# Kernel tuning notes

Measured on AMD Instinct MI355X. Metric: run time of the kernel, lower is better.

## Reference

```python
import jax, jax.numpy as jnp
import numpy as np

FACTOR = 1.0
MARGIN = 0.5
NUM_CLASS = 19


def setup_inputs() -> dict:
    key = jax.random.key(0)
    k1, k2, k3 = jax.random.split(key, 3)
    B, C, H, W = 8, 256, 128, 128
    features = jax.random.normal(k1, (B, C, H, W), dtype=jnp.float32)
    labels = jax.random.randint(k2, (B, H, W), 0, NUM_CLASS, dtype=jnp.int32)
    prototypes = jax.random.normal(k3, (NUM_CLASS, C), dtype=jnp.float32)
    return {"features": features, "labels": labels, "prototypes": prototypes}


def reference(features, labels, prototypes):
    b, c, h, w = features.shape
    # flatten to [N, C] pixels and [N] labels (labels already at (h, w))
    feat = jnp.transpose(features, (0, 2, 3, 1)).reshape(-1, c)
    lab = labels.reshape(-1)
    # per-class mean via one-pass segment reduce (all classes present)
    sums = jax.ops.segment_sum(feat, lab, num_segments=NUM_CLASS)          # [K, C]
    counts = jax.ops.segment_sum(jnp.ones_like(lab, feat.dtype), lab,
                                 num_segments=NUM_CLASS)                   # [K]
    means = sums / jnp.maximum(counts, 1.0)[:, None]
    # L2 normalize (torch F.normalize uses eps=1e-12 clamp on the norm)
    norms = jnp.maximum(jnp.linalg.norm(means, axis=1, keepdims=True), 1e-12)
    mn = means / norms
    # pairwise cosine distance, diagonal forced to 2.0
    D = 1.0 - mn @ mn.T                                                    # [K, K]
    D = jnp.where(jnp.eye(NUM_CLASS, dtype=bool), 2.0, D)
    loss = jnp.mean(jnp.maximum(MARGIN - D, 0.0))
    return FACTOR * loss
```

## Files before the change

### kernel.cpp

```cpp
#include <hip/hip_runtime.h>
#include <hip/hip_bf16.h>

namespace {

constexpr int K  = 19;
constexpr int C  = 256;
constexpr int HW = 16384;
constexpr int B  = 8;

__global__ __launch_bounds__(256) void fsl_accum(const float* __restrict__ feat,
                                                 const int* __restrict__ labels,
                                                 float* __restrict__ psums,
                                                 float* __restrict__ pcounts) {
    __shared__ float acc[4][K][64];
    __shared__ int   cnt[4][32];
    const int tid  = threadIdx.x;
    const int lane = tid & 63;
    const int w    = tid >> 6;
    const int c    = blockIdx.x;
    const int b    = blockIdx.y;
    const bool do_count = (c == 0);

    for (int i = tid; i < 4 * K * 64; i += 256) ((float*)acc)[i] = 0.f;
    if (tid < 128) ((int*)cnt)[tid] = 0;
    __syncthreads();

    const float* fp = feat + (size_t)(b * C + c) * HW;
    const int*   lp = labels + (size_t)b * HW;
    float* mya = &acc[w][0][lane];

    #pragma unroll 4
    for (int it = 0; it < HW / 1024; ++it) {
        const int px  = it * 1024 + tid * 4;
        const float4 v  = *(const float4*)(fp + px);
        const int4   lb = *(const int4*)(lp + px);
        mya[lb.x * 64] += v.x;
        mya[lb.y * 64] += v.y;
        mya[lb.z * 64] += v.z;
        mya[lb.w * 64] += v.w;
        if (do_count) {
            atomicAdd(&cnt[w][lb.x], 1);
            atomicAdd(&cnt[w][lb.y], 1);
            atomicAdd(&cnt[w][lb.z], 1);
            atomicAdd(&cnt[w][lb.w], 1);
        }
    }
    __syncthreads();

    for (int idx = tid; idx < K * 64; idx += 256) {
        const int k = idx >> 6, l = idx & 63;
        acc[0][k][l] = acc[0][k][l] + acc[1][k][l] + acc[2][k][l] + acc[3][k][l];
    }
    __syncthreads();

    for (int k = w; k < K; k += 4) {
        float v = acc[0][k][lane];
        v += __shfl_down(v, 32);
        v += __shfl_down(v, 16);
        v += __shfl_down(v, 8);
        v += __shfl_down(v, 4);
        v += __shfl_down(v, 2);
        v += __shfl_down(v, 1);
        if (lane == 0) psums[((size_t)b * K + k) * C + c] = v;
    }
    if (do_count && tid < K) {
        pcounts[b * K + tid] =
            (float)(cnt[0][tid] + cnt[1][tid] + cnt[2][tid] + cnt[3][tid]);
    }
}

__global__ __launch_bounds__(384) void fsl_finalize(const float* __restrict__ psums,
                                                    const float* __restrict__ pcounts,
                                                    float* __restrict__ out) {
    __shared__ float mm[K][260];
    __shared__ float rcount[K];
    __shared__ float norm2s[K];
    __shared__ float rnorm[K];
    __shared__ float wred[6];
    const int tid = threadIdx.x;

    if (tid < K) {
        float cc = 0.f;
        #pragma unroll
        for (int b = 0; b < B; ++b) cc += pcounts[b * K + tid];
        rcount[tid] = 1.0f / fmaxf(cc, 1.0f);
    }
    __syncthreads();

    if (tid < C) {
        #pragma unroll
        for (int k = 0; k < K; ++k) {
            float s = 0.f;
            #pragma unroll
            for (int b = 0; b < B; ++b) s += psums[((size_t)b * K + k) * C + tid];
            mm[k][tid] = s * rcount[k];
        }
    }
    __syncthreads();

    if (tid < K * 16) {
        const int k = tid >> 4, sub = tid & 15;
        float s = 0.f;
        #pragma unroll
        for (int j = 0; j < 16; ++j) {
            const float v = mm[k][sub + j * 16];
            s += v * v;
        }
        s += __shfl_xor(s, 8);
        s += __shfl_xor(s, 4);
        s += __shfl_xor(s, 2);
        s += __shfl_xor(s, 1);
        if (sub == 0) norm2s[k] = s;
    }
    __syncthreads();
    if (tid < K) rnorm[tid] = 1.0f / fmaxf(sqrtf(norm2s[tid]), 1e-12f);
    __syncthreads();

    float contrib = 0.f;
    if (tid < K * K) {
        const int i = tid / K;
        const int j = tid - i * K;
        const float4* ri = (const float4*)&mm[i][0];
        const float4* rj = (const float4*)&mm[j][0];
        float dot = 0.f;
        #pragma unroll 8
        for (int q = 0; q < C / 4; ++q) {
            const float4 a = ri[q], bv = rj[q];
            dot += a.x * bv.x + a.y * bv.y + a.z * bv.z + a.w * bv.w;
        }
        const float g = dot * rnorm[i] * rnorm[j];
        contrib = (i == j) ? 0.f : fmaxf(g - 0.5f, 0.f);
    }

    float v = contrib;
    v += __shfl_down(v, 32);
    v += __shfl_down(v, 16);
    v += __shfl_down(v, 8);
    v += __shfl_down(v, 4);
    v += __shfl_down(v, 2);
    v += __shfl_down(v, 1);
    if ((tid & 63) == 0) wred[tid >> 6] = v;
    __syncthreads();
    if (tid == 0) {
        float t = 0.f;
        #pragma unroll
        for (int q = 0; q < 6; ++q) t += wred[q];
        out[0] = 1.0f * t / (float)(K * K);
    }
}

}

extern "C" void kernel_launch(void* const* d_in, const int* in_sizes, int n_in,
                              void* d_out, int out_size, void* d_ws, size_t ws_size,
                              hipStream_t stream) {
    const float* feat   = (const float*)d_in[0];
    const int*   labels = (const int*)d_in[1];

    float* psums   = (float*)d_ws;
    float* pcounts = psums + B * K * C;
    float* out     = (float*)d_out;

    dim3 gridA(C, B);
    fsl_accum<<<gridA, 256, 0, stream>>>(feat, labels, psums, pcounts);
    fsl_finalize<<<1, 384, 0, stream>>>(psums, pcounts, out);
}
```

Measured before the change: 200.5 us.

## Split label counting into dedicated blocks and use nontemporal feature loads

Label counting moves out of the channel-0 blocks, which previously did extra LDS atomics, into 8 dedicated blocks that count with per-lane float accumulators. This removes the straggler blocks that made the c==0 column slower than the rest. The grid is flattened to 1D with b as the fast index, so neighbouring blocks read different batches. Feature loads become nontemporal because the data is streamed once. Counting in float is exact at these sizes.

```diff
diff --git a/kernel.cpp b/kernel.cpp
--- a/kernel.cpp
+++ b/kernel.cpp
@@ -8,42 +8,68 @@
 constexpr int HW = 16384;
 constexpr int B  = 8;
 
+typedef float f4 __attribute__((ext_vector_type(4)));
+typedef int   i4 __attribute__((ext_vector_type(4)));
+
 __global__ __launch_bounds__(256) void fsl_accum(const float* __restrict__ feat,
                                                  const int* __restrict__ labels,
                                                  float* __restrict__ psums,
                                                  float* __restrict__ pcounts) {
     __shared__ float acc[4][K][64];
-    __shared__ int   cnt[4][32];
     const int tid  = threadIdx.x;
     const int lane = tid & 63;
     const int w    = tid >> 6;
-    const int c    = blockIdx.x;
-    const int b    = blockIdx.y;
-    const bool do_count = (c == 0);
+    const int id   = blockIdx.x;
 
     for (int i = tid; i < 4 * K * 64; i += 256) ((float*)acc)[i] = 0.f;
-    if (tid < 128) ((int*)cnt)[tid] = 0;
     __syncthreads();
 
+    float* mya = &acc[w][0][lane];
+
+    if (id < 8) {
+        const int b = id;
+        const int* lp = labels + (size_t)b * HW;
+        #pragma unroll 4
+        for (int it = 0; it < HW / 1024; ++it) {
+            const i4 lb = *(const i4*)(lp + it * 1024 + tid * 4);
+            mya[lb.x * 64] += 1.f;
+            mya[lb.y * 64] += 1.f;
+            mya[lb.z * 64] += 1.f;
+            mya[lb.w * 64] += 1.f;
+        }
+        __syncthreads();
+        for (int idx = tid; idx < K * 64; idx += 256) {
+            const int k = idx >> 6, l = idx & 63;
+            acc[0][k][l] = acc[0][k][l] + acc[1][k][l] + acc[2][k][l] + acc[3][k][l];
+        }
+        __syncthreads();
+        for (int k = w; k < K; k += 4) {
+            float v = acc[0][k][lane];
+            v += __shfl_down(v, 32);
+            v += __shfl_down(v, 16);
+            v += __shfl_down(v, 8);
+            v += __shfl_down(v, 4);
+            v += __shfl_down(v, 2);
+            v += __shfl_down(v, 1);
+            if (lane == 0) pcounts[b * K + k] = v;
+        }
+        return;
+    }
+
+    const int b = (id - 8) & 7;
+    const int c = (id - 8) >> 3;
     const float* fp = feat + (size_t)(b * C + c) * HW;
     const int*   lp = labels + (size_t)b * HW;
-    float* mya = &acc[w][0][lane];
 
     #pragma unroll 4
     for (int it = 0; it < HW / 1024; ++it) {
-        const int px  = it * 1024 + tid * 4;
-        const float4 v  = *(const float4*)(fp + px);
-        const int4   lb = *(const int4*)(lp + px);
+        const int px = it * 1024 + tid * 4;
+        const f4 v  = __builtin_nontemporal_load((const f4*)(fp + px));
+        const i4 lb = *(const i4*)(lp + px);
         mya[lb.x * 64] += v.x;
         mya[lb.y * 64] += v.y;
         mya[lb.z * 64] += v.z;
         mya[lb.w * 64] += v.w;
-        if (do_count) {
-            atomicAdd(&cnt[w][lb.x], 1);
-            atomicAdd(&cnt[w][lb.y], 1);
-            atomicAdd(&cnt[w][lb.z], 1);
-            atomicAdd(&cnt[w][lb.w], 1);
-        }
     }
     __syncthreads();
 
@@ -62,10 +88,6 @@
         v += __shfl_down(v, 2);
         v += __shfl_down(v, 1);
         if (lane == 0) psums[((size_t)b * K + k) * C + c] = v;
-    }
-    if (do_count && tid < K) {
-        pcounts[b * K + tid] =
-            (float)(cnt[0][tid] + cnt[1][tid] + cnt[2][tid] + cnt[3][tid]);
     }
 }
 
@@ -161,7 +183,6 @@
     float* pcounts = psums + B * K * C;
     float* out     = (float*)d_out;
 
-    dim3 gridA(C, B);
-    fsl_accum<<<gridA, 256, 0, stream>>>(feat, labels, psums, pcounts);
+    fsl_accum<<<8 + C * B, 256, 0, stream>>>(feat, labels, psums, pcounts);
     fsl_finalize<<<1, 384, 0, stream>>>(psums, pcounts, out);
 }
```

After: 192.0 us. -4.3%, faster.
